# Kernel optimization log

Hardware: AMD Instinct MI355X
Metric: run time of the kernel (lower is better)

The kernel has to match this reference:

```python
import jax, jax.numpy as jnp
import numpy as np

B, S, H, NH = 2, 2048, 1024, 16
HD = H // NH

def setup_inputs() -> dict:
    key = jax.random.key(0)
    ks = jax.random.split(key, 10)
    f = lambda k, shape, scale: jax.random.normal(k, shape, dtype=jnp.float32) * scale
    return {
        "hidden_states": f(ks[0], (B, S, H), 1.0),
        "attention_mask": f(ks[1], (B, 1, S, S), 1.0),
        # static weights: randn * static_ratio(0.9); dynamic: randn * 0.01
        "q_static": f(ks[2], (H, H), 0.9), "q_dynamic": f(ks[3], (H, H), 0.01),
        "k_static": f(ks[4], (H, H), 0.9), "k_dynamic": f(ks[5], (H, H), 0.01),
        "v_static": f(ks[6], (H, H), 0.9), "v_dynamic": f(ks[7], (H, H), 0.01),
        "o_static": f(ks[8], (H, H), 0.9), "o_dynamic": f(ks[9], (H, H), 0.01),
    }

def _split_heads(x):
    # [B, S, H] -> [B, NH, S, HD]
    b, s, _ = x.shape
    return x.reshape(b, s, NH, HD).transpose(0, 2, 1, 3)

def reference(hidden_states, attention_mask,
              q_static, q_dynamic, k_static, k_dynamic,
              v_static, v_dynamic, o_static, o_dynamic):
    # DualWeightLinear: y = x @ (static + dynamic)^T  (no bias)
    q = hidden_states @ (q_static + q_dynamic).T
    k = hidden_states @ (k_static + k_dynamic).T
    v = hidden_states @ (v_static + v_dynamic).T
    q, k, v = _split_heads(q), _split_heads(k), _split_heads(v)  # [B,NH,S,HD]
    scale = 1.0 / np.sqrt(HD).astype(np.float32)
    scores = jnp.einsum('bhqd,bhkd->bhqk', q, k) * scale  # [B,NH,S,S]
    scores = scores + attention_mask  # additive mask, broadcast over heads
    attn = jax.nn.softmax(scores, axis=-1)
    out = jnp.einsum('bhqk,bhkd->bhqd', attn, v)
    out = out.transpose(0, 2, 1, 3).reshape(hidden_states.shape[0], hidden_states.shape[1], H)
    return out @ (o_static + o_dynamic).T
```

## Files before the change

### kernel.cpp

```cpp
#include <hip/hip_runtime.h>
#include <hip/hip_bf16.h>
#include <stdint.h>

#define BB 2
#define SS 2048
#define HH 1024
#define NHH 16
#define HDD 64
#define MM (BB*SS)
#define N4SEG (HH*HH/4)

typedef __attribute__((ext_vector_type(8))) short short8;
typedef __attribute__((ext_vector_type(4))) float f32x4;
typedef __attribute__((ext_vector_type(4))) unsigned short u16x4;

__device__ __forceinline__ unsigned short f2bf(float x){
  unsigned u = __float_as_uint(x);
  u += 0x7fffu + ((u >> 16) & 1u);
  return (unsigned short)(u >> 16);
}
__device__ __forceinline__ float bf2f(unsigned short h){
  return __uint_as_float(((unsigned)h) << 16);
}
__device__ __forceinline__ unsigned short f2bf_fast(float x){
  __hip_bfloat16 hb = __float2bfloat16(x);
  return *reinterpret_cast<unsigned short*>(&hb);
}

__global__ void k_split(const float* __restrict__ in, unsigned short* __restrict__ hi,
                        unsigned short* __restrict__ lo, int n4){
  int i = blockIdx.x * blockDim.x + threadIdx.x;
  if (i >= n4) return;
  f32x4 x = ((const f32x4*)in)[i];
  u16x4 h, l;
  #pragma unroll
  for (int j = 0; j < 4; ++j){
    unsigned short hb = f2bf(x[j]);
    h[j] = hb;
    l[j] = f2bf(x[j] - bf2f(hb));
  }
  ((u16x4*)hi)[i] = h;
  ((u16x4*)lo)[i] = l;
}

__global__ void k_wprep(const float* __restrict__ qs, const float* __restrict__ qd,
                        const float* __restrict__ ks, const float* __restrict__ kd,
                        const float* __restrict__ vs, const float* __restrict__ vd,
                        const float* __restrict__ os_, const float* __restrict__ od,
                        unsigned short* __restrict__ wqh, unsigned short* __restrict__ wql,
                        unsigned short* __restrict__ wkh, unsigned short* __restrict__ wkl,
                        unsigned short* __restrict__ wv,  unsigned short* __restrict__ wo){
  int i = blockIdx.x * blockDim.x + threadIdx.x;
  int seg = i >> 18;
  int j = i & (N4SEG - 1);
  const float *pa, *pb; unsigned short *ph, *pl = nullptr;
  if      (seg == 0){ pa = qs; pb = qd; ph = wqh; pl = wql; }
  else if (seg == 1){ pa = ks; pb = kd; ph = wkh; pl = wkl; }
  else if (seg == 2){ pa = vs; pb = vd; ph = wv; }
  else              { pa = os_; pb = od; ph = wo; }
  f32x4 x = ((const f32x4*)pa)[j] + ((const f32x4*)pb)[j];
  u16x4 h, l;
  #pragma unroll
  for (int c = 0; c < 4; ++c){
    unsigned short hb = f2bf(x[c]);
    h[c] = hb;
    l[c] = f2bf(x[c] - bf2f(hb));
  }
  ((u16x4*)ph)[j] = h;
  if (pl) ((u16x4*)pl)[j] = l;
}

__global__ void k_maskperm(const float* __restrict__ m, float* __restrict__ pm){
  int i = blockIdx.x * blockDim.x + threadIdx.x;
  int lr = i & 15;
  int q  = (i >> 4) & 2047;
  int t  = (i >> 15) & 31;
  int b  = i >> 20;
  const float* src = m + ((size_t)(b*2048 + q))*2048 + t*64 + lr;
  f32x4 v = { src[0], src[16], src[32], src[48] };
  ((f32x4*)pm)[i] = v;
}

__global__ __launch_bounds__(256, 2)
void proj_fused(const unsigned short* __restrict__ hsh, const unsigned short* __restrict__ hsl,
                const unsigned short* __restrict__ wqh, const unsigned short* __restrict__ wql,
                const unsigned short* __restrict__ wkh, const unsigned short* __restrict__ wkl,
                const unsigned short* __restrict__ wv,
                unsigned short* __restrict__ qhB, unsigned short* __restrict__ qlB,
                unsigned short* __restrict__ khB, unsigned short* __restrict__ klB,
                unsigned short* __restrict__ vtB)
{
  __shared__ unsigned short Ash[128*32], Asl[128*32], Bsh[128*32], Bsl[128*32];
  const int tid = threadIdx.x;
  const int nb0 = blockIdx.x * 128;
  const int mb0 = blockIdx.y * 128;
  const int kind = nb0 >> 10;
  const int ncol0 = nb0 & 1023;
  const int w  = tid >> 6, lane = tid & 63;
  const int wr = w >> 1,  wc = w & 1;
  const int lg = lane >> 4, lr = lane & 15;

  const unsigned short* Bh = (kind == 0 ? wqh : (kind == 1 ? wkh : wv)) + (size_t)ncol0 * HH;
  const unsigned short* Bl = (kind == 0 ? wql : wkl) + (size_t)ncol0 * HH;
  const unsigned short* Ahb = hsh + (size_t)mb0 * HH;
  const unsigned short* Alb = hsl + (size_t)mb0 * HH;

  f32x4 zero4 = {0.f, 0.f, 0.f, 0.f};
  f32x4 acc[4][4];
  #pragma unroll
  for (int mi = 0; mi < 4; ++mi)
    #pragma unroll
    for (int ni = 0; ni < 4; ++ni) acc[mi][ni] = zero4;

  for (int kb = 0; kb < HH; kb += 32) {
    __syncthreads();
    #pragma unroll
    for (int i = 0; i < 2; ++i){
      int c = i*256 + tid;
      int row = c >> 2, off = (c & 3) << 3;
      size_t go = (size_t)row * HH + kb + off;
      __builtin_amdgcn_global_load_lds(
          (const __attribute__((address_space(1))) void*)(Ahb + go),
          (__attribute__((address_space(3))) void*)(&Ash[c*8]), 16, 0, 0);
      __builtin_amdgcn_global_load_lds(
          (const __attribute__((address_space(1))) void*)(Alb + go),
          (__attribute__((address_space(3))) void*)(&Asl[c*8]), 16, 0, 0);
      __builtin_amdgcn_global_load_lds(
          (const __attribute__((address_space(1))) void*)(Bh + go),
          (__attribute__((address_space(3))) void*)(&Bsh[c*8]), 16, 0, 0);
      if (kind < 2)
        __builtin_amdgcn_global_load_lds(
            (const __attribute__((address_space(1))) void*)(Bl + go),
            (__attribute__((address_space(3))) void*)(&Bsl[c*8]), 16, 0, 0);
    }
    __syncthreads();
    short8 ah4[4], al4[4], bh4[4], bl4[4];
    #pragma unroll
    for (int mi = 0; mi < 4; ++mi){
      int ro = (wr*64 + mi*16 + lr)*32 + lg*8;
      ah4[mi] = *(const short8*)&Ash[ro];
      al4[mi] = *(const short8*)&Asl[ro];
    }
    #pragma unroll
    for (int ni = 0; ni < 4; ++ni){
      int ro = (wc*64 + ni*16 + lr)*32 + lg*8;
      bh4[ni] = *(const short8*)&Bsh[ro];
    }
    if (kind < 2) {
      #pragma unroll
      for (int ni = 0; ni < 4; ++ni){
        int ro = (wc*64 + ni*16 + lr)*32 + lg*8;
        bl4[ni] = *(const short8*)&Bsl[ro];
      }
      #pragma unroll
      for (int mi = 0; mi < 4; ++mi)
        #pragma unroll
        for (int ni = 0; ni < 4; ++ni){
          acc[mi][ni] = __builtin_amdgcn_mfma_f32_16x16x32_bf16(ah4[mi], bh4[ni], acc[mi][ni], 0, 0, 0);
          acc[mi][ni] = __builtin_amdgcn_mfma_f32_16x16x32_bf16(al4[mi], bh4[ni], acc[mi][ni], 0, 0, 0);
          acc[mi][ni] = __builtin_amdgcn_mfma_f32_16x16x32_bf16(ah4[mi], bl4[ni], acc[mi][ni], 0, 0, 0);
        }
    } else {
      #pragma unroll
      for (int mi = 0; mi < 4; ++mi)
        #pragma unroll
        for (int ni = 0; ni < 4; ++ni)
          acc[mi][ni] = __builtin_amdgcn_mfma_f32_16x16x32_bf16(ah4[mi], bh4[ni], acc[mi][ni], 0, 0, 0);
    }
  }

  if (kind == 2) {
    #pragma unroll
    for (int mi = 0; mi < 4; ++mi){
      #pragma unroll
      for (int ni = 0; ni < 4; ++ni){
        int nv = ncol0 + wc*64 + ni*16 + lr;
        int m0 = mb0 + wr*64 + mi*16 + 4*lg;
        int b = m0 >> 11, s0 = m0 & 2047;
        u16x4 pk;
        #pragma unroll
        for (int r = 0; r < 4; ++r) pk[r] = f2bf_fast(acc[mi][ni][r]);
        *(u16x4*)&vtB[((size_t)(b*HH + nv))*SS + s0] = pk;
      }
    }
  } else {
    unsigned short* Ch = (kind == 0) ? qhB : khB;
    unsigned short* Cl = (kind == 0) ? qlB : klB;
    #pragma unroll
    for (int mi = 0; mi < 4; ++mi){
      #pragma unroll
      for (int ni = 0; ni < 4; ++ni){
        int n  = ncol0 + wc*64 + ni*16 + lr;
        int m0 = mb0 + wr*64 + mi*16 + 4*lg;
        #pragma unroll
        for (int r = 0; r < 4; ++r){
          float x = acc[mi][ni][r];
          unsigned short hb = f2bf(x);
          unsigned short lb = f2bf(x - bf2f(hb));
          size_t o = (size_t)(m0 + r)*HH + n;
          Ch[o] = hb;
          Cl[o] = lb;
        }
      }
    }
  }
}

__global__ __launch_bounds__(256, 2)
void gemm_o(const unsigned short* __restrict__ A, const unsigned short* __restrict__ Bm,
            float* __restrict__ C, int M, int N, int K)
{
  __shared__ unsigned short As[128*32];
  __shared__ unsigned short Bs[128*32];
  const int tid = threadIdx.x;
  const int mb0 = blockIdx.y * 128, nb0 = blockIdx.x * 128;
  const int w  = tid >> 6, lane = tid & 63;
  const int wr = w >> 1,  wc = w & 1;
  const int lg = lane >> 4, lr = lane & 15;

  f32x4 zero4 = {0.f, 0.f, 0.f, 0.f};
  f32x4 acc[4][4];
  #pragma unroll
  for (int mi = 0; mi < 4; ++mi)
    #pragma unroll
    for (int ni = 0; ni < 4; ++ni) acc[mi][ni] = zero4;

  const unsigned short* Abase = A  + (size_t)mb0 * K;
  const unsigned short* Bbase = Bm + (size_t)nb0 * K;

  for (int kb = 0; kb < K; kb += 32) {
    __syncthreads();
    #pragma unroll
    for (int i = 0; i < 2; ++i){
      int c = i*256 + tid;
      int row = c >> 2, off = (c & 3) << 3;
      size_t go = (size_t)row * K + kb + off;
      __builtin_amdgcn_global_load_lds(
          (const __attribute__((address_space(1))) void*)(Abase + go),
          (__attribute__((address_space(3))) void*)(&As[c*8]), 16, 0, 0);
      __builtin_amdgcn_global_load_lds(
          (const __attribute__((address_space(1))) void*)(Bbase + go),
          (__attribute__((address_space(3))) void*)(&Bs[c*8]), 16, 0, 0);
    }
    __syncthreads();
    short8 af[4], bfr[4];
    #pragma unroll
    for (int mi = 0; mi < 4; ++mi) af[mi]  = *(const short8*)&As[(wr*64 + mi*16 + lr)*32 + lg*8];
    #pragma unroll
    for (int ni = 0; ni < 4; ++ni) bfr[ni] = *(const short8*)&Bs[(wc*64 + ni*16 + lr)*32 + lg*8];
    #pragma unroll
    for (int mi = 0; mi < 4; ++mi)
      #pragma unroll
      for (int ni = 0; ni < 4; ++ni)
        acc[mi][ni] = __builtin_amdgcn_mfma_f32_16x16x32_bf16(af[mi], bfr[ni], acc[mi][ni], 0, 0, 0);
  }

  #pragma unroll
  for (int mi = 0; mi < 4; ++mi){
    #pragma unroll
    for (int ni = 0; ni < 4; ++ni){
      int n  = nb0 + wc*64 + ni*16 + lr;
      int m0 = mb0 + wr*64 + mi*16 + 4*lg;
      #pragma unroll
      for (int r = 0; r < 4; ++r) C[(size_t)(m0 + r)*N + n] = acc[mi][ni][r];
    }
  }
}

__global__ __launch_bounds__(512, 4)
void attn_fwd(const unsigned short* __restrict__ qh, const unsigned short* __restrict__ ql,
              const unsigned short* __restrict__ kh, const unsigned short* __restrict__ kl,
              const unsigned short* __restrict__ vt, const float* __restrict__ pm,
              unsigned short* __restrict__ ao)
{
  __shared__ unsigned short Ksh[2][64*64];
  __shared__ unsigned short Ksl[2][64*64];
  __shared__ unsigned short Vss[2][64*64];
  __shared__ unsigned short P[8][16*64];

  const int tid = threadIdx.x;
  const int w = tid >> 6, lane = tid & 63;
  const int lg = lane >> 4, lr = lane & 15;
  const int xork = (lr & 7) << 4;

  const int bid = (blockIdx.x & 7) * 64 + (blockIdx.x >> 3);
  const int qb = bid & 15, h = (bid >> 4) & 15, b = bid >> 8;
  const int q0 = qb*128 + w*16;
  const int hoff = h*64;

  const int srow = tid >> 3;
  const int sgx  = (tid & 7) ^ (srow & 7);

  short8 qfh[2], qfl[2];
  {
    size_t qoff = ((size_t)(b*SS + q0 + lr))*HH + hoff + lg*8;
    qfh[0] = *(const short8*)(qh + qoff);
    qfl[0] = *(const short8*)(ql + qoff);
    qfh[1] = *(const short8*)(qh + qoff + 32);
    qfl[1] = *(const short8*)(ql + qoff + 32);
  }
  short8 ones8;
  #pragma unroll
  for (int j = 0; j < 8; ++j) ones8[j] = (short)0x3F80;

  float m_run[4] = {-1e30f, -1e30f, -1e30f, -1e30f};
  f32x4 zero4 = {0.f, 0.f, 0.f, 0.f};
  f32x4 acc[4], acc_l = zero4;
  #pragma unroll
  for (int d4 = 0; d4 < 4; ++d4) acc[d4] = zero4;

  const float* mbase = pm + ((size_t)b*32*2048 + q0 + 4*lg)*64 + (size_t)lr*4;

  #define ATTN_STAGE(buf, kvb) do {                                              \
    size_t kro = ((size_t)(b*SS + (kvb) + srow))*HH + hoff + sgx*8;              \
    size_t vro = ((size_t)(b*HH + hoff + srow))*SS + (kvb) + sgx*8;              \
    __builtin_amdgcn_global_load_lds(                                            \
        (const __attribute__((address_space(1))) void*)(kh + kro),               \
        (__attribute__((address_space(3))) void*)(&Ksh[buf][tid*8]), 16, 0, 0);  \
    __builtin_amdgcn_global_load_lds(                                            \
        (const __attribute__((address_space(1))) void*)(kl + kro),               \
        (__attribute__((address_space(3))) void*)(&Ksl[buf][tid*8]), 16, 0, 0);  \
    __builtin_amdgcn_global_load_lds(                                            \
        (const __attribute__((address_space(1))) void*)(vt + vro),               \
        (__attribute__((address_space(3))) void*)(&Vss[buf][tid*8]), 16, 0, 0);  \
  } while (0)

  ATTN_STAGE(0, 0);

  for (int t = 0; t < SS/64; ++t) {
    const int kv = t*64;
    const int cur = t & 1;
    __syncthreads();
    if (t + 1 < SS/64) ATTN_STAGE(cur ^ 1, kv + 64);

    const float* mp = mbase + (size_t)t*(2048*64);
    f32x4 mk4[4];
    #pragma unroll
    for (int r = 0; r < 4; ++r) mk4[r] = *(const f32x4*)(mp + r*64);

    f32x4 sc[4];
    const int c0 = ((0  + lg*16) ^ xork) >> 1;
    const int c1 = ((64 + lg*16) ^ xork) >> 1;
    #pragma unroll
    for (int nb = 0; nb < 4; ++nb) {
      const int krow = (nb*16 + lr)*64;
      short8 k0h = *(const short8*)&Ksh[cur][krow + c0];
      short8 k1h = *(const short8*)&Ksh[cur][krow + c1];
      short8 k0l = *(const short8*)&Ksl[cur][krow + c0];
      short8 k1l = *(const short8*)&Ksl[cur][krow + c1];
      f32x4 d = zero4;
      d = __builtin_amdgcn_mfma_f32_16x16x32_bf16(qfh[0], k0h, d, 0, 0, 0);
      d = __builtin_amdgcn_mfma_f32_16x16x32_bf16(qfh[1], k1h, d, 0, 0, 0);
      d = __builtin_amdgcn_mfma_f32_16x16x32_bf16(qfh[0], k0l, d, 0, 0, 0);
      d = __builtin_amdgcn_mfma_f32_16x16x32_bf16(qfh[1], k1l, d, 0, 0, 0);
      d = __builtin_amdgcn_mfma_f32_16x16x32_bf16(qfl[0], k0h, d, 0, 0, 0);
      d = __builtin_amdgcn_mfma_f32_16x16x32_bf16(qfl[1], k1h, d, 0, 0, 0);
      sc[nb] = d;
    }

    float s[4][4], rmax[4];
    #pragma unroll
    for (int r = 0; r < 4; ++r) {
      float a0 = fmaf(sc[0][r], 0.125f, mk4[r][0]);
      float a1 = fmaf(sc[1][r], 0.125f, mk4[r][1]);
      float a2 = fmaf(sc[2][r], 0.125f, mk4[r][2]);
      float a3 = fmaf(sc[3][r], 0.125f, mk4[r][3]);
      s[0][r] = a0; s[1][r] = a1; s[2][r] = a2; s[3][r] = a3;
      rmax[r] = fmaxf(fmaxf(a0, a1), fmaxf(a2, a3));
    }
    #pragma unroll
    for (int off = 1; off < 16; off <<= 1) {
      #pragma unroll
      for (int r = 0; r < 4; ++r) rmax[r] = fmaxf(rmax[r], __shfl_xor(rmax[r], off, 16));
    }
    float corr[4];
    #pragma unroll
    for (int r = 0; r < 4; ++r) {
      float mn = fmaxf(m_run[r], rmax[r]);
      corr[r] = __expf(m_run[r] - mn);
      m_run[r] = mn;
      const int prow = 4*lg + r;
      const int pxor = (prow & 7) << 4;
      #pragma unroll
      for (int nb = 0; nb < 4; ++nb) {
        float pv = __expf(s[nb][r] - mn);
        P[w][prow*64 + (((((nb*16 + lr) << 1)) ^ pxor) >> 1)] = f2bf_fast(pv);
      }
    }
    #pragma unroll
    for (int d4 = 0; d4 < 4; ++d4)
      #pragma unroll
      for (int r = 0; r < 4; ++r) acc[d4][r] *= corr[r];
    #pragma unroll
    for (int r = 0; r < 4; ++r) acc_l[r] *= corr[r];

    const int p0 = c0, p1 = c1;
    short8 pf0 = *(const short8*)&P[w][lr*64 + p0];
    short8 pf1 = *(const short8*)&P[w][lr*64 + p1];
    acc_l = __builtin_amdgcn_mfma_f32_16x16x32_bf16(pf0, ones8, acc_l, 0, 0, 0);
    acc_l = __builtin_amdgcn_mfma_f32_16x16x32_bf16(pf1, ones8, acc_l, 0, 0, 0);
    #pragma unroll
    for (int d4 = 0; d4 < 4; ++d4) {
      const int vrow = (d4*16 + lr)*64;
      short8 vf0 = *(const short8*)&Vss[cur][vrow + p0];
      short8 vf1 = *(const short8*)&Vss[cur][vrow + p1];
      acc[d4] = __builtin_amdgcn_mfma_f32_16x16x32_bf16(pf0, vf0, acc[d4], 0, 0, 0);
      acc[d4] = __builtin_amdgcn_mfma_f32_16x16x32_bf16(pf1, vf1, acc[d4], 0, 0, 0);
    }
  }
  #undef ATTN_STAGE

  float inv[4];
  #pragma unroll
  for (int r = 0; r < 4; ++r) inv[r] = 1.0f / acc_l[r];
  #pragma unroll
  for (int d4 = 0; d4 < 4; ++d4)
    #pragma unroll
    for (int r = 0; r < 4; ++r) {
      size_t o = ((size_t)(b*SS + q0 + 4*lg + r))*HH + hoff + d4*16 + lr;
      ao[o] = f2bf_fast(acc[d4][r] * inv[r]);
    }
}

extern "C" void kernel_launch(void* const* d_in, const int* in_sizes, int n_in,
                              void* d_out, int out_size, void* d_ws, size_t ws_size,
                              hipStream_t stream)
{
  const float* hs  = (const float*)d_in[0];
  const float* msk = (const float*)d_in[1];
  const float* qs  = (const float*)d_in[2];
  const float* qd  = (const float*)d_in[3];
  const float* ks  = (const float*)d_in[4];
  const float* kd  = (const float*)d_in[5];
  const float* vs  = (const float*)d_in[6];
  const float* vd  = (const float*)d_in[7];
  const float* os_ = (const float*)d_in[8];
  const float* od  = (const float*)d_in[9];
  float* out = (float*)d_out;

  const size_t NHS = (size_t)MM * HH;
  const size_t NW  = (size_t)HH * HH;
  unsigned short* p = (unsigned short*)d_ws;
  unsigned short* hsh = p; p += NHS;
  unsigned short* hsl = p; p += NHS;
  unsigned short* wqh = p; p += NW;
  unsigned short* wql = p; p += NW;
  unsigned short* wkh = p; p += NW;
  unsigned short* wkl = p; p += NW;
  unsigned short* wv  = p; p += NW;
  unsigned short* wo  = p; p += NW;
  unsigned short* qhB = p; p += NHS;
  unsigned short* qlB = p; p += NHS;
  unsigned short* khB = p; p += NHS;
  unsigned short* klB = p; p += NHS;
  unsigned short* vtB = p; p += NHS;
  unsigned short* aoB = p; p += NHS;
  float* pm = (float*)p;

  k_split   <<<(int)(NHS/1024), 256, 0, stream>>>(hs, hsh, hsl, (int)(NHS/4));
  k_wprep   <<<(int)(4*N4SEG/256), 256, 0, stream>>>(qs, qd, ks, kd, vs, vd, os_, od,
                                                     wqh, wql, wkh, wkl, wv, wo);
  k_maskperm<<<8192, 256, 0, stream>>>(msk, pm);

  proj_fused<<<dim3(3*HH/128, MM/128), 256, 0, stream>>>(hsh, hsl, wqh, wql, wkh, wkl, wv,
                                                         qhB, qlB, khB, klB, vtB);

  attn_fwd<<<BB*NHH*(SS/128), 512, 0, stream>>>(qhB, qlB, khB, klB, vtB, pm, aoB);

  gemm_o<<<dim3(HH/128, MM/128), 256, 0, stream>>>(aoB, wo, out, MM, HH, HH);
}
```

Measured before the change: 353.7 us.

## Compute transposed scores to read mask directly and pass P via bpermute

```diff
diff --git a/kernel.cpp b/kernel.cpp
--- a/kernel.cpp
+++ b/kernel.cpp
@@ -13,6 +13,7 @@
 typedef __attribute__((ext_vector_type(8))) short short8;
 typedef __attribute__((ext_vector_type(4))) float f32x4;
 typedef __attribute__((ext_vector_type(4))) unsigned short u16x4;
+typedef __attribute__((ext_vector_type(4))) unsigned int u32x4;
 
 __device__ __forceinline__ unsigned short f2bf(float x){
   unsigned u = __float_as_uint(x);
@@ -68,17 +69,6 @@
   }
   ((u16x4*)ph)[j] = h;
   if (pl) ((u16x4*)pl)[j] = l;
-}
-
-__global__ void k_maskperm(const float* __restrict__ m, float* __restrict__ pm){
-  int i = blockIdx.x * blockDim.x + threadIdx.x;
-  int lr = i & 15;
-  int q  = (i >> 4) & 2047;
-  int t  = (i >> 15) & 31;
-  int b  = i >> 20;
-  const float* src = m + ((size_t)(b*2048 + q))*2048 + t*64 + lr;
-  f32x4 v = { src[0], src[16], src[32], src[48] };
-  ((f32x4*)pm)[i] = v;
 }
 
 __global__ __launch_bounds__(256, 2)
@@ -270,13 +260,12 @@
 __global__ __launch_bounds__(512, 4)
 void attn_fwd(const unsigned short* __restrict__ qh, const unsigned short* __restrict__ ql,
               const unsigned short* __restrict__ kh, const unsigned short* __restrict__ kl,
-              const unsigned short* __restrict__ vt, const float* __restrict__ pm,
+              const unsigned short* __restrict__ vt, const float* __restrict__ mask,
               unsigned short* __restrict__ ao)
 {
   __shared__ unsigned short Ksh[2][64*64];
   __shared__ unsigned short Ksl[2][64*64];
   __shared__ unsigned short Vss[2][64*64];
-  __shared__ unsigned short P[8][16*64];
 
   const int tid = threadIdx.x;
   const int w = tid >> 6, lane = tid & 63;
@@ -290,6 +279,12 @@
 
   const int srow = tid >> 3;
   const int sgx  = (tid & 7) ^ (srow & 7);
+
+  const int aLO = ((lg & 1)*32 + lr) * 4;
+  const int aHI = aLO + 64;
+  int addr_c[4];
+  #pragma unroll
+  for (int r = 0; r < 4; ++r) addr_c[r] = (lg*20 + r) * 4;
 
   short8 qfh[2], qfl[2];
   {
@@ -303,13 +298,13 @@
   #pragma unroll
   for (int j = 0; j < 8; ++j) ones8[j] = (short)0x3F80;
 
-  float m_run[4] = {-1e30f, -1e30f, -1e30f, -1e30f};
+  float m_run = -1e30f;
   f32x4 zero4 = {0.f, 0.f, 0.f, 0.f};
   f32x4 acc[4], acc_l = zero4;
   #pragma unroll
   for (int d4 = 0; d4 < 4; ++d4) acc[d4] = zero4;
 
-  const float* mbase = pm + ((size_t)b*32*2048 + q0 + 4*lg)*64 + (size_t)lr*4;
+  const float* mrow = mask + ((size_t)(b*SS + q0 + lr))*SS + 4*lg;
 
   #define ATTN_STAGE(buf, kvb) do {                                              \
     size_t kro = ((size_t)(b*SS + (kvb) + srow))*HH + hoff + sgx*8;              \
@@ -333,14 +328,13 @@
     __syncthreads();
     if (t + 1 < SS/64) ATTN_STAGE(cur ^ 1, kv + 64);
 
-    const float* mp = mbase + (size_t)t*(2048*64);
-    f32x4 mk4[4];
-    #pragma unroll
-    for (int r = 0; r < 4; ++r) mk4[r] = *(const f32x4*)(mp + r*64);
-
-    f32x4 sc[4];
+    f32x4 mk[4];
+    #pragma unroll
+    for (int nb = 0; nb < 4; ++nb) mk[nb] = *(const f32x4*)(mrow + kv + nb*16);
+
     const int c0 = ((0  + lg*16) ^ xork) >> 1;
     const int c1 = ((64 + lg*16) ^ xork) >> 1;
+    f32x4 sc[4];
     #pragma unroll
     for (int nb = 0; nb < 4; ++nb) {
       const int krow = (nb*16 + lr)*64;
@@ -349,61 +343,92 @@
       short8 k0l = *(const short8*)&Ksl[cur][krow + c0];
       short8 k1l = *(const short8*)&Ksl[cur][krow + c1];
       f32x4 d = zero4;
-      d = __builtin_amdgcn_mfma_f32_16x16x32_bf16(qfh[0], k0h, d, 0, 0, 0);
-      d = __builtin_amdgcn_mfma_f32_16x16x32_bf16(qfh[1], k1h, d, 0, 0, 0);
-      d = __builtin_amdgcn_mfma_f32_16x16x32_bf16(qfh[0], k0l, d, 0, 0, 0);
-      d = __builtin_amdgcn_mfma_f32_16x16x32_bf16(qfh[1], k1l, d, 0, 0, 0);
-      d = __builtin_amdgcn_mfma_f32_16x16x32_bf16(qfl[0], k0h, d, 0, 0, 0);
-      d = __builtin_amdgcn_mfma_f32_16x16x32_bf16(qfl[1], k1h, d, 0, 0, 0);
+      d = __builtin_amdgcn_mfma_f32_16x16x32_bf16(k0h, qfh[0], d, 0, 0, 0);
+      d = __builtin_amdgcn_mfma_f32_16x16x32_bf16(k1h, qfh[1], d, 0, 0, 0);
+      d = __builtin_amdgcn_mfma_f32_16x16x32_bf16(k0l, qfh[0], d, 0, 0, 0);
+      d = __builtin_amdgcn_mfma_f32_16x16x32_bf16(k1l, qfh[1], d, 0, 0, 0);
+      d = __builtin_amdgcn_mfma_f32_16x16x32_bf16(k0h, qfl[0], d, 0, 0, 0);
+      d = __builtin_amdgcn_mfma_f32_16x16x32_bf16(k1h, qfl[1], d, 0, 0, 0);
       sc[nb] = d;
     }
 
-    float s[4][4], rmax[4];
+    float s[4][4];
+    float rmax = -1e30f;
+    #pragma unroll
+    for (int nb = 0; nb < 4; ++nb)
+      #pragma unroll
+      for (int r = 0; r < 4; ++r) {
+        float v = fmaf(sc[nb][r], 0.125f, mk[nb][r]);
+        s[nb][r] = v;
+        rmax = fmaxf(rmax, v);
+      }
+    rmax = fmaxf(rmax, __shfl_xor(rmax, 16));
+    rmax = fmaxf(rmax, __shfl_xor(rmax, 32));
+
+    float mn = fmaxf(m_run, rmax);
+    float corr = __expf(m_run - mn);
+    m_run = mn;
     #pragma unroll
     for (int r = 0; r < 4; ++r) {
-      float a0 = fmaf(sc[0][r], 0.125f, mk4[r][0]);
-      float a1 = fmaf(sc[1][r], 0.125f, mk4[r][1]);
-      float a2 = fmaf(sc[2][r], 0.125f, mk4[r][2]);
-      float a3 = fmaf(sc[3][r], 0.125f, mk4[r][3]);
-      s[0][r] = a0; s[1][r] = a1; s[2][r] = a2; s[3][r] = a3;
-      rmax[r] = fmaxf(fmaxf(a0, a1), fmaxf(a2, a3));
-    }
-    #pragma unroll
-    for (int off = 1; off < 16; off <<= 1) {
-      #pragma unroll
-      for (int r = 0; r < 4; ++r) rmax[r] = fmaxf(rmax[r], __shfl_xor(rmax[r], off, 16));
-    }
-    float corr[4];
-    #pragma unroll
-    for (int r = 0; r < 4; ++r) {
-      float mn = fmaxf(m_run[r], rmax[r]);
-      corr[r] = __expf(m_run[r] - mn);
-      m_run[r] = mn;
-      const int prow = 4*lg + r;
-      const int pxor = (prow & 7) << 4;
-      #pragma unroll
-      for (int nb = 0; nb < 4; ++nb) {
-        float pv = __expf(s[nb][r] - mn);
-        P[w][prow*64 + (((((nb*16 + lr) << 1)) ^ pxor) >> 1)] = f2bf_fast(pv);
-      }
-    }
-    #pragma unroll
-    for (int d4 = 0; d4 < 4; ++d4)
-      #pragma unroll
-      for (int r = 0; r < 4; ++r) acc[d4][r] *= corr[r];
-    #pragma unroll
-    for (int r = 0; r < 4; ++r) acc_l[r] *= corr[r];
-
-    const int p0 = c0, p1 = c1;
-    short8 pf0 = *(const short8*)&P[w][lr*64 + p0];
-    short8 pf1 = *(const short8*)&P[w][lr*64 + p1];
+      float ca = __int_as_float(
+          __builtin_amdgcn_ds_bpermute(addr_c[r], __float_as_int(corr)));
+      acc_l[r] *= ca;
+      #pragma unroll
+      for (int d4 = 0; d4 < 4; ++d4) acc[d4][r] *= ca;
+    }
+
+    unsigned pw[4][2];
+    #pragma unroll
+    for (int nb = 0; nb < 4; ++nb) {
+      float e0 = __expf(s[nb][0] - m_run);
+      float e1 = __expf(s[nb][1] - m_run);
+      float e2 = __expf(s[nb][2] - m_run);
+      float e3 = __expf(s[nb][3] - m_run);
+      pw[nb][0] = (unsigned)f2bf(e0) | ((unsigned)f2bf(e1) << 16);
+      pw[nb][1] = (unsigned)f2bf(e2) | ((unsigned)f2bf(e3) << 16);
+    }
+
+    const int B0 = lg >> 1;
+    u32x4 f0, f1;
+    {
+      unsigned g0 = __builtin_amdgcn_ds_bpermute(aLO, (int)pw[0][0]);
+      unsigned g1 = __builtin_amdgcn_ds_bpermute(aLO, (int)pw[0][1]);
+      unsigned g2 = __builtin_amdgcn_ds_bpermute(aLO, (int)pw[1][0]);
+      unsigned g3 = __builtin_amdgcn_ds_bpermute(aLO, (int)pw[1][1]);
+      unsigned g4 = __builtin_amdgcn_ds_bpermute(aHI, (int)pw[0][0]);
+      unsigned g5 = __builtin_amdgcn_ds_bpermute(aHI, (int)pw[0][1]);
+      unsigned g6 = __builtin_amdgcn_ds_bpermute(aHI, (int)pw[1][0]);
+      unsigned g7 = __builtin_amdgcn_ds_bpermute(aHI, (int)pw[1][1]);
+      f0[0] = B0 ? g2 : g0;
+      f0[1] = B0 ? g3 : g1;
+      f0[2] = B0 ? g6 : g4;
+      f0[3] = B0 ? g7 : g5;
+    }
+    {
+      unsigned g0 = __builtin_amdgcn_ds_bpermute(aLO, (int)pw[2][0]);
+      unsigned g1 = __builtin_amdgcn_ds_bpermute(aLO, (int)pw[2][1]);
+      unsigned g2 = __builtin_amdgcn_ds_bpermute(aLO, (int)pw[3][0]);
+      unsigned g3 = __builtin_amdgcn_ds_bpermute(aLO, (int)pw[3][1]);
+      unsigned g4 = __builtin_amdgcn_ds_bpermute(aHI, (int)pw[2][0]);
+      unsigned g5 = __builtin_amdgcn_ds_bpermute(aHI, (int)pw[2][1]);
+      unsigned g6 = __builtin_amdgcn_ds_bpermute(aHI, (int)pw[3][0]);
+      unsigned g7 = __builtin_amdgcn_ds_bpermute(aHI, (int)pw[3][1]);
+      f1[0] = B0 ? g2 : g0;
+      f1[1] = B0 ? g3 : g1;
+      f1[2] = B0 ? g6 : g4;
+      f1[3] = B0 ? g7 : g5;
+    }
+    short8 pf0 = *reinterpret_cast<short8*>(&f0);
+    short8 pf1 = *reinterpret_cast<short8*>(&f1);
+
     acc_l = __builtin_amdgcn_mfma_f32_16x16x32_bf16(pf0, ones8, acc_l, 0, 0, 0);
     acc_l = __builtin_amdgcn_mfma_f32_16x16x32_bf16(pf1, ones8, acc_l, 0, 0, 0);
+
     #pragma unroll
     for (int d4 = 0; d4 < 4; ++d4) {
       const int vrow = (d4*16 + lr)*64;
-      short8 vf0 = *(const short8*)&Vss[cur][vrow + p0];
-      short8 vf1 = *(const short8*)&Vss[cur][vrow + p1];
+      short8 vf0 = *(const short8*)&Vss[cur][vrow + c0];
+      short8 vf1 = *(const short8*)&Vss[cur][vrow + c1];
       acc[d4] = __builtin_amdgcn_mfma_f32_16x16x32_bf16(pf0, vf0, acc[d4], 0, 0, 0);
       acc[d4] = __builtin_amdgcn_mfma_f32_16x16x32_bf16(pf1, vf1, acc[d4], 0, 0, 0);
     }
@@ -455,17 +480,15 @@
   unsigned short* klB = p; p += NHS;
   unsigned short* vtB = p; p += NHS;
   unsigned short* aoB = p; p += NHS;
-  float* pm = (float*)p;
-
-  k_split   <<<(int)(NHS/1024), 256, 0, stream>>>(hs, hsh, hsl, (int)(NHS/4));
-  k_wprep   <<<(int)(4*N4SEG/256), 256, 0, stream>>>(qs, qd, ks, kd, vs, vd, os_, od,
-                                                     wqh, wql, wkh, wkl, wv, wo);
-  k_maskperm<<<8192, 256, 0, stream>>>(msk, pm);
+
+  k_split<<<(int)(NHS/1024), 256, 0, stream>>>(hs, hsh, hsl, (int)(NHS/4));
+  k_wprep<<<(int)(4*N4SEG/256), 256, 0, stream>>>(qs, qd, ks, kd, vs, vd, os_, od,
+                                                  wqh, wql, wkh, wkl, wv, wo);
 
   proj_fused<<<dim3(3*HH/128, MM/128), 256, 0, stream>>>(hsh, hsl, wqh, wql, wkh, wkl, wv,
                                                          qhB, qlB, khB, klB, vtB);
 
-  attn_fwd<<<BB*NHH*(SS/128), 512, 0, stream>>>(qhB, qlB, khB, klB, vtB, pm, aoB);
+  attn_fwd<<<BB*NHH*(SS/128), 512, 0, stream>>>(qhB, qlB, khB, klB, vtB, msk, aoB);
 
   gemm_o<<<dim3(HH/128, MM/128), 256, 0, stream>>>(aoB, wo, out, MM, HH, HH);
 }
```

After: 332.2 us. 1.06x faster.
